# Kernel tuning notes

Hardware: AMD Instinct MI355X
Metric: run time of the kernel (lower is better)

The kernel has to match this reference:

```python
import jax, jax.numpy as jnp
import numpy as np

OUT = 7          # output_size
SR = 2           # sampling_ratio
CANON_SIZE = 224.0
CANON_LVL = 4
MIN_LVL, MAX_LVL = 2, 5
SCALES = (0.25, 0.125, 0.0625, 0.03125)
IMG = 1024.0


def _roi_align(feat, batch_idx, boxes, scale):
    """ROIAlign aligned=True. feat [B,C,H,W], boxes [R,4] (x1,y1,x2,y2) in image coords.
    Returns [R,C,OUT,OUT]."""
    B, C, H, W = feat.shape
    R = boxes.shape[0]
    x1 = boxes[:, 0] * scale - 0.5
    y1 = boxes[:, 1] * scale - 0.5
    x2 = boxes[:, 2] * scale - 0.5
    y2 = boxes[:, 3] * scale - 0.5
    bin_w = (x2 - x1) / OUT
    bin_h = (y2 - y1) / OUT
    S = OUT * SR
    # sample positions in bin units: bin p, sub-sample i -> p + (i+0.5)/SR
    g = (jnp.arange(S, dtype=feat.dtype) + 0.5) / SR
    ys = y1[:, None] + g[None, :] * bin_h[:, None]   # [R,S]
    xs = x1[:, None] + g[None, :] * bin_w[:, None]   # [R,S]
    vy = (ys >= -1.0) & (ys <= H)
    vx = (xs >= -1.0) & (xs <= W)
    yc = jnp.clip(ys, 0.0, H - 1)
    xc = jnp.clip(xs, 0.0, W - 1)
    y0 = jnp.floor(yc).astype(jnp.int32)
    x0 = jnp.floor(xc).astype(jnp.int32)
    y1i = jnp.minimum(y0 + 1, H - 1)
    x1i = jnp.minimum(x0 + 1, W - 1)
    ly = yc - y0.astype(feat.dtype); hy = 1.0 - ly
    lx = xc - x0.astype(feat.dtype); hx = 1.0 - lx
    f = jnp.transpose(feat, (0, 2, 3, 1))            # [B,H,W,C]
    b = batch_idx[:, None, None]                     # [R,1,1]

    def gather(yi, xi):
        # advanced indexing broadcast -> [R,S,S,C]
        return f[b, yi[:, :, None], xi[:, None, :], :]

    def w2(wy, wx):
        return (wy[:, :, None] * wx[:, None, :])[..., None]

    v = (gather(y0, x0) * w2(hy, hx)
         + gather(y0, x1i) * w2(hy, lx)
         + gather(y1i, x0) * w2(ly, hx)
         + gather(y1i, x1i) * w2(ly, lx))             # [R,S,S,C]
    mask = (vy[:, :, None] & vx[:, None, :])[..., None]
    v = jnp.where(mask, v, jnp.zeros((), feat.dtype))
    v = v.reshape(R, OUT, SR, OUT, SR, C).mean(axis=(2, 4))  # avg over SRxSR samples
    return jnp.transpose(v, (0, 3, 1, 2))            # [R,C,OUT,OUT]


def setup_inputs() -> dict:
    key = jax.random.key(0)
    k2, k3, k4, k5, kwh, kc = jax.random.split(key, 6)
    B, C, N = 2, 256, 256
    x2 = jax.random.normal(k2, (B, C, 256, 256), jnp.float32)
    x3 = jax.random.normal(k3, (B, C, 128, 128), jnp.float32)
    x4 = jax.random.normal(k4, (B, C, 64, 64), jnp.float32)
    x5 = jax.random.normal(k5, (B, C, 32, 32), jnp.float32)
    wh = jax.random.uniform(kwh, (B, N, 2), jnp.float32, 32.0, 480.0)
    cxy = jax.random.uniform(kc, (B, N, 2), jnp.float32, 0.0, IMG)
    p1 = jnp.clip(cxy - wh / 2, 0.0, IMG)
    p2 = jnp.clip(cxy + wh / 2, 0.0, IMG)
    boxes = jnp.concatenate([p1, p2], axis=-1)  # [B,N,4] = (x1,y1,x2,y2)
    return {"x2": x2, "x3": x3, "x4": x4, "x5": x5, "boxes": boxes}


def reference(x2, x3, x4, x5, boxes):
    B, N, _ = boxes.shape
    flat = boxes.reshape(B * N, 4)
    batch_idx = jnp.repeat(jnp.arange(B, dtype=jnp.int32), N)
    # FPN level assignment
    area = (flat[:, 2] - flat[:, 0]) * (flat[:, 3] - flat[:, 1])
    sizes = jnp.sqrt(area)
    lvl = jnp.floor(CANON_LVL + jnp.log2(sizes / CANON_SIZE + 1e-8))
    lvl = jnp.clip(lvl, MIN_LVL, MAX_LVL).astype(jnp.int32) - MIN_LVL  # [R] in {0..3}
    feats = (x2, x3, x4, x5)
    C = x2.shape[1]
    out = jnp.zeros((B * N, C, OUT, OUT), x2.dtype)
    for l, (f, s) in enumerate(zip(feats, SCALES)):
        pooled = _roi_align(f, batch_idx, flat, s)
        out = jnp.where((lvl == l)[:, None, None, None], pooled, out)
    return out
```

## Files before the change

### kernel.cpp

```cpp
#include <hip/hip_runtime.h>


#define OUTD 7
#define SRD  2
#define SD   14
#define CCH  256
#define NBOX 256
#define NC   4
#define NCHK (CCH / NC)
#define CAPU 345
#define CAPF (CAPU * 4)
#define NBIN (OUTD * OUTD)

typedef __attribute__((address_space(1))) unsigned int gu32;
typedef __attribute__((address_space(3))) unsigned int lu32;

__device__ __forceinline__ void gl2lds16(const float* g, float* l) {
    __builtin_amdgcn_global_load_lds((gu32*)(unsigned long long)g, (lu32*)l, 16, 0, 0);
}

__global__ __launch_bounds__(256) void roi_direct(
    const float* __restrict__ f0, const float* __restrict__ f1,
    const float* __restrict__ f2, const float* __restrict__ f3,
    const float* __restrict__ boxes, float* __restrict__ out)
{
    const int roi = blockIdx.x;
    const int c0  = blockIdx.y * NC;
    const int t   = threadIdx.x;
    const int b   = roi / NBOX;

    const float bx1 = boxes[roi * 4 + 0];
    const float by1 = boxes[roi * 4 + 1];
    const float bx2 = boxes[roi * 4 + 2];
    const float by2 = boxes[roi * 4 + 3];

    const float area = (bx2 - bx1) * (by2 - by1);
    const float sz   = sqrtf(area);
    int lvl = (int)floorf(4.0f + log2f(sz * (1.0f / 224.0f) + 1e-8f));
    lvl = min(max(lvl, 2), 5) - 2;

    const int   wsh   = 8 - lvl;
    const int   H     = 1 << wsh;
    const int   W     = H;
    const float scale = 1.0f / (float)(4 << lvl);
    const size_t HW   = (size_t)1 << (2 * wsh);

    const float* f  = (lvl == 0) ? f0 : (lvl == 1) ? f1 : (lvl == 2) ? f2 : f3;
    const float* fb = f + (size_t)b * CCH * HW;

    __shared__ int   s_ax0[SD], s_ax1[SD], s_ay0[SD], s_ay1[SD];
    __shared__ float s_wxh[SD], s_wxl[SD], s_wyh[SD], s_wyl[SD];
    __shared__ __align__(16) float s_win[NC * CAPF];

    if (t < SD) {
        const int i = t;
        const float x1r = bx1 * scale - 0.5f;
        const float y1r = by1 * scale - 0.5f;
        const float x2r = bx2 * scale - 0.5f;
        const float y2r = by2 * scale - 0.5f;
        const float bw = (x2r - x1r) * (1.0f / OUTD);
        const float bh = (y2r - y1r) * (1.0f / OUTD);
        const float g  = ((float)i + 0.5f) * (1.0f / SRD);
        const float ys = y1r + g * bh;
        const float xs = x1r + g * bw;
        const float vy = ((ys >= -1.0f) && (ys <= (float)H)) ? 1.0f : 0.0f;
        const float vx = ((xs >= -1.0f) && (xs <= (float)W)) ? 1.0f : 0.0f;
        const float yc = fminf(fmaxf(ys, 0.0f), (float)(H - 1));
        const float xc = fminf(fmaxf(xs, 0.0f), (float)(W - 1));
        const int y0 = (int)yc;
        const int x0 = (int)xc;
        const float ly = yc - (float)y0;
        const float lx = xc - (float)x0;
        s_ay0[i] = y0;
        s_ay1[i] = min(y0 + 1, H - 1);
        s_ax0[i] = x0;
        s_ax1[i] = min(x0 + 1, W - 1);
        s_wyh[i] = vy * (1.0f - ly);
        s_wyl[i] = vy * ly;
        s_wxh[i] = vx * (1.0f - lx);
        s_wxl[i] = vx * lx;
    }
    __syncthreads();

    const int y_lo = s_ay0[0];
    const int y_hi = s_ay1[SD - 1];
    const int x_lo = s_ax0[0] & ~3;
    const int x_hi = s_ax1[SD - 1];
    const int W4 = (x_hi - x_lo + 4) >> 2;
    const int Hw = y_hi - y_lo + 1;
    const int L4 = Hw * W4;

    const int ci  = t / NBIN;
    const int bin = t - ci * NBIN;
    const int oy  = bin / 7;
    const int ox  = bin - oy * 7;
    const int ia = 2 * oy, ib = ia + 1;
    const int ja = 2 * ox, jb = ja + 1;

    float* ob = out + (size_t)roi * (CCH * NBIN) + (size_t)c0 * NBIN;

    if (L4 <= CAPU) {
        const float invW4 = 1.0f / (float)W4;
        const int wv = t >> 6, ln = t & 63;
        const unsigned int gmax = (512u << (2 * wsh)) - 4u;
        const unsigned int wbase = ((unsigned int)y_lo << wsh) + (unsigned int)x_lo;
        for (int c = 0; c < NC; ++c) {
            const unsigned int ch_base =
                (((unsigned int)(b * CCH + c0 + c)) << (2 * wsh)) + wbase;
            float* lb = s_win + c * CAPF;
            for (int o0 = ((wv + c) & 3) << 6; o0 < L4; o0 += 256) {
                const int u = o0 + ln;
                if (u < L4) {
                    int y  = (int)((float)u * invW4);
                    int x4 = u - y * W4;
                    if (x4 < 0)        { x4 += W4; --y; }
                    else if (x4 >= W4) { x4 -= W4; ++y; }
                    unsigned int g = ch_base + ((unsigned int)y << wsh) + ((unsigned int)x4 << 2);
                    g = min(g, gmax);
                    gl2lds16(f + g, lb + (o0 << 2));
                }
            }
        }
        __syncthreads();

        if (t < NC * NBIN) {
            const int rs = W4 << 2;
            const int ryA0 = (s_ay0[ia] - y_lo) * rs, ryA1 = (s_ay1[ia] - y_lo) * rs;
            const int ryB0 = (s_ay0[ib] - y_lo) * rs, ryB1 = (s_ay1[ib] - y_lo) * rs;
            const int rxA0 = s_ax0[ja] - x_lo,        rxA1 = s_ax1[ja] - x_lo;
            const int rxB0 = s_ax0[jb] - x_lo,        rxB1 = s_ax1[jb] - x_lo;
            const float wyAh = s_wyh[ia], wyAl = s_wyl[ia];
            const float wyBh = s_wyh[ib], wyBl = s_wyl[ib];
            const float wxAh = s_wxh[ja], wxAl = s_wxl[ja];
            const float wxBh = s_wxh[jb], wxBl = s_wxl[jb];
            const float* w = s_win + ci * CAPF;
            const float acc =
                wyAh * (wxAh * w[ryA0 + rxA0] + wxAl * w[ryA0 + rxA1])
              + wyAl * (wxAh * w[ryA1 + rxA0] + wxAl * w[ryA1 + rxA1])
              + wyAh * (wxBh * w[ryA0 + rxB0] + wxBl * w[ryA0 + rxB1])
              + wyAl * (wxBh * w[ryA1 + rxB0] + wxBl * w[ryA1 + rxB1])
              + wyBh * (wxAh * w[ryB0 + rxA0] + wxAl * w[ryB0 + rxA1])
              + wyBl * (wxAh * w[ryB1 + rxA0] + wxAl * w[ryB1 + rxA1])
              + wyBh * (wxBh * w[ryB0 + rxB0] + wxBl * w[ryB0 + rxB1])
              + wyBl * (wxBh * w[ryB1 + rxB0] + wxBl * w[ryB1 + rxB1]);
            ob[t] = acc * 0.25f;
        }
    } else {
        if (t < NC * NBIN) {
            const float* fc = fb + (size_t)(c0 + ci) * HW;
            const float acc =
                s_wyh[ia] * (s_wxh[ja] * fc[s_ay0[ia] * W + s_ax0[ja]] + s_wxl[ja] * fc[s_ay0[ia] * W + s_ax1[ja]])
              + s_wyl[ia] * (s_wxh[ja] * fc[s_ay1[ia] * W + s_ax0[ja]] + s_wxl[ja] * fc[s_ay1[ia] * W + s_ax1[ja]])
              + s_wyh[ia] * (s_wxh[jb] * fc[s_ay0[ia] * W + s_ax0[jb]] + s_wxl[jb] * fc[s_ay0[ia] * W + s_ax1[jb]])
              + s_wyl[ia] * (s_wxh[jb] * fc[s_ay1[ia] * W + s_ax0[jb]] + s_wxl[jb] * fc[s_ay1[ia] * W + s_ax1[jb]])
              + s_wyh[ib] * (s_wxh[ja] * fc[s_ay0[ib] * W + s_ax0[ja]] + s_wxl[ja] * fc[s_ay0[ib] * W + s_ax1[ja]])
              + s_wyl[ib] * (s_wxh[ja] * fc[s_ay1[ib] * W + s_ax0[ja]] + s_wxl[ja] * fc[s_ay1[ib] * W + s_ax1[ja]])
              + s_wyh[ib] * (s_wxh[jb] * fc[s_ay0[ib] * W + s_ax0[jb]] + s_wxl[jb] * fc[s_ay0[ib] * W + s_ax1[jb]])
              + s_wyl[ib] * (s_wxh[jb] * fc[s_ay1[ib] * W + s_ax0[jb]] + s_wxl[jb] * fc[s_ay1[ib] * W + s_ax1[jb]]);
            ob[t] = acc * 0.25f;
        }
    }
}

extern "C" void kernel_launch(void* const* d_in, const int* in_sizes, int n_in,
                              void* d_out, int out_size, void* d_ws, size_t ws_size,
                              hipStream_t stream) {
    const float* f0    = (const float*)d_in[0];
    const float* f1    = (const float*)d_in[1];
    const float* f2    = (const float*)d_in[2];
    const float* f3    = (const float*)d_in[3];
    const float* boxes = (const float*)d_in[4];
    float*       outp  = (float*)d_out;

    const int R = out_size / (CCH * NBIN);
    roi_direct<<<dim3(R, NCHK), 256, 0, stream>>>(f0, f1, f2, f3, boxes, outp);
}
```

Measured before the change: 263.6 us.

## Process 16 channels per block with smaller LDS window and no sync

Raises channels per block from 4 to 16 and shrinks the LDS window capacity so up to 128 float4 loads per channel are issued from precomputed offsets. The window bounds are now computed redundantly in every thread, which removes one barrier. The fallback path computes sample coordinates inline instead of reading shared tables. This cuts the grid size and amortises per-block setup across more channels. In exchange, fewer ROIs fit in the LDS path and more of them take the direct global-gather path.

```diff
diff --git a/kernel.cpp b/kernel.cpp
--- a/kernel.cpp
+++ b/kernel.cpp
@@ -2,15 +2,15 @@
 
 
 #define OUTD 7
-#define SRD  2
 #define SD   14
 #define CCH  256
 #define NBOX 256
-#define NC   4
+#define NC   16
 #define NCHK (CCH / NC)
-#define CAPU 345
+#define CAPU 76
 #define CAPF (CAPU * 4)
 #define NBIN (OUTD * OUTD)
+#define NOUT (NC * NBIN)
 
 typedef __attribute__((address_space(1))) unsigned int gu32;
 typedef __attribute__((address_space(3))) unsigned int lu32;
@@ -27,7 +27,7 @@
     const int roi = blockIdx.x;
     const int c0  = blockIdx.y * NC;
     const int t   = threadIdx.x;
-    const int b   = roi / NBOX;
+    const int b   = roi >> 8;
 
     const float bx1 = boxes[roi * 4 + 0];
     const float by1 = boxes[roi * 4 + 1];
@@ -48,116 +48,135 @@
     const float* f  = (lvl == 0) ? f0 : (lvl == 1) ? f1 : (lvl == 2) ? f2 : f3;
     const float* fb = f + (size_t)b * CCH * HW;
 
-    __shared__ int   s_ax0[SD], s_ax1[SD], s_ay0[SD], s_ay1[SD];
-    __shared__ float s_wxh[SD], s_wxl[SD], s_wyh[SD], s_wyl[SD];
+    __shared__ int2   s_py[SD], s_px[SD];
+    __shared__ float2 s_wy[SD], s_wx[SD];
     __shared__ __align__(16) float s_win[NC * CAPF];
+
+    const float x1r = bx1 * scale - 0.5f;
+    const float y1r = by1 * scale - 0.5f;
+    const float bw  = (bx2 - bx1) * scale * (1.0f / OUTD);
+    const float bh  = (by2 - by1) * scale * (1.0f / OUTD);
+    const float Wm1 = (float)(W - 1);
+
+    const float xs0  = x1r + 0.25f * bw, xs13 = x1r + 6.75f * bw;
+    const float ys0  = y1r + 0.25f * bh, ys13 = y1r + 6.75f * bh;
+    const int xf = (int)fminf(fmaxf(xs0, 0.0f), Wm1);
+    const int yf = (int)fminf(fmaxf(ys0, 0.0f), Wm1);
+    const int xl = min((int)fminf(fmaxf(xs13, 0.0f), Wm1) + 1, W - 1);
+    const int yl = min((int)fminf(fmaxf(ys13, 0.0f), Wm1) + 1, W - 1);
+    const int x_lo = xf & ~3;
+    const int y_lo = yf;
+    const int W4 = (xl - x_lo + 4) >> 2;
+    const int Hw = yl - y_lo + 1;
+    const int L4 = Hw * W4;
+    const int rs = W4 << 2;
 
     if (t < SD) {
         const int i = t;
-        const float x1r = bx1 * scale - 0.5f;
-        const float y1r = by1 * scale - 0.5f;
-        const float x2r = bx2 * scale - 0.5f;
-        const float y2r = by2 * scale - 0.5f;
-        const float bw = (x2r - x1r) * (1.0f / OUTD);
-        const float bh = (y2r - y1r) * (1.0f / OUTD);
-        const float g  = ((float)i + 0.5f) * (1.0f / SRD);
+        const float g  = ((float)i + 0.5f) * 0.5f;
         const float ys = y1r + g * bh;
         const float xs = x1r + g * bw;
         const float vy = ((ys >= -1.0f) && (ys <= (float)H)) ? 1.0f : 0.0f;
         const float vx = ((xs >= -1.0f) && (xs <= (float)W)) ? 1.0f : 0.0f;
-        const float yc = fminf(fmaxf(ys, 0.0f), (float)(H - 1));
-        const float xc = fminf(fmaxf(xs, 0.0f), (float)(W - 1));
+        const float yc = fminf(fmaxf(ys, 0.0f), Wm1);
+        const float xc = fminf(fmaxf(xs, 0.0f), Wm1);
         const int y0 = (int)yc;
         const int x0 = (int)xc;
         const float ly = yc - (float)y0;
         const float lx = xc - (float)x0;
-        s_ay0[i] = y0;
-        s_ay1[i] = min(y0 + 1, H - 1);
-        s_ax0[i] = x0;
-        s_ax1[i] = min(x0 + 1, W - 1);
-        s_wyh[i] = vy * (1.0f - ly);
-        s_wyl[i] = vy * ly;
-        s_wxh[i] = vx * (1.0f - lx);
-        s_wxl[i] = vx * lx;
+        s_py[i] = make_int2((y0 - y_lo) * rs, (min(y0 + 1, H - 1) - y_lo) * rs);
+        s_px[i] = make_int2(x0 - x_lo, min(x0 + 1, W - 1) - x_lo);
+        s_wy[i] = make_float2(vy * (1.0f - ly), vy * ly);
+        s_wx[i] = make_float2(vx * (1.0f - lx), vx * lx);
     }
-    __syncthreads();
-
-    const int y_lo = s_ay0[0];
-    const int y_hi = s_ay1[SD - 1];
-    const int x_lo = s_ax0[0] & ~3;
-    const int x_hi = s_ax1[SD - 1];
-    const int W4 = (x_hi - x_lo + 4) >> 2;
-    const int Hw = y_hi - y_lo + 1;
-    const int L4 = Hw * W4;
-
-    const int ci  = t / NBIN;
-    const int bin = t - ci * NBIN;
-    const int oy  = bin / 7;
-    const int ox  = bin - oy * 7;
-    const int ia = 2 * oy, ib = ia + 1;
-    const int ja = 2 * ox, jb = ja + 1;
 
     float* ob = out + (size_t)roi * (CCH * NBIN) + (size_t)c0 * NBIN;
 
     if (L4 <= CAPU) {
+        const int wv = t >> 6, ln = t & 63;
+        const int nT2 = (L4 > 64) ? 1 : 0;
         const float invW4 = 1.0f / (float)W4;
-        const int wv = t >> 6, ln = t & 63;
-        const unsigned int gmax = (512u << (2 * wsh)) - 4u;
+
+        int yA = (int)((float)ln * invW4);
+        int xA = ln - yA * W4;
+        if (xA < 0) { xA += W4; --yA; } else if (xA >= W4) { xA -= W4; ++yA; }
+        const int offA = (yA << wsh) + (xA << 2);
+        int yB = (int)((float)(ln + 64) * invW4);
+        int xB = (ln + 64) - yB * W4;
+        if (xB < 0) { xB += W4; --yB; } else if (xB >= W4) { xB -= W4; ++yB; }
+        const int offB = (yB << wsh) + (xB << 2);
+
         const unsigned int wbase = ((unsigned int)y_lo << wsh) + (unsigned int)x_lo;
-        for (int c = 0; c < NC; ++c) {
-            const unsigned int ch_base =
-                (((unsigned int)(b * CCH + c0 + c)) << (2 * wsh)) + wbase;
-            float* lb = s_win + c * CAPF;
-            for (int o0 = ((wv + c) & 3) << 6; o0 < L4; o0 += 256) {
-                const int u = o0 + ln;
-                if (u < L4) {
-                    int y  = (int)((float)u * invW4);
-                    int x4 = u - y * W4;
-                    if (x4 < 0)        { x4 += W4; --y; }
-                    else if (x4 >= W4) { x4 -= W4; ++y; }
-                    unsigned int g = ch_base + ((unsigned int)y << wsh) + ((unsigned int)x4 << 2);
-                    g = min(g, gmax);
-                    gl2lds16(f + g, lb + (o0 << 2));
-                }
+        const unsigned int cb0   = ((unsigned int)(b * CCH + c0) << (2 * wsh)) + wbase;
+        const unsigned int gmax  = (512u << (2 * wsh)) - 4u;
+        const int nIt = NC << nT2;
+        for (int it = wv; it < nIt; it += 4) {
+            const int c  = it >> nT2;
+            const int tl = it & nT2;
+            const int off = tl ? offB : offA;
+            if (ln + (tl << 6) < L4) {
+                unsigned int g = cb0 + ((unsigned int)c << (2 * wsh)) + (unsigned int)off;
+                g = min(g, gmax);
+                gl2lds16(f + g, s_win + c * CAPF + (tl << 8));
             }
         }
         __syncthreads();
 
-        if (t < NC * NBIN) {
-            const int rs = W4 << 2;
-            const int ryA0 = (s_ay0[ia] - y_lo) * rs, ryA1 = (s_ay1[ia] - y_lo) * rs;
-            const int ryB0 = (s_ay0[ib] - y_lo) * rs, ryB1 = (s_ay1[ib] - y_lo) * rs;
-            const int rxA0 = s_ax0[ja] - x_lo,        rxA1 = s_ax1[ja] - x_lo;
-            const int rxB0 = s_ax0[jb] - x_lo,        rxB1 = s_ax1[jb] - x_lo;
-            const float wyAh = s_wyh[ia], wyAl = s_wyl[ia];
-            const float wyBh = s_wyh[ib], wyBl = s_wyl[ib];
-            const float wxAh = s_wxh[ja], wxAl = s_wxl[ja];
-            const float wxBh = s_wxh[jb], wxBl = s_wxl[jb];
+        for (int idx = t; idx < NOUT; idx += 256) {
+            const int ci  = idx / NBIN;
+            const int bin = idx - ci * NBIN;
+            const int oy  = bin / 7;
+            const int ox  = bin - oy * 7;
+            const int ia = 2 * oy, ib = ia + 1;
+            const int ja = 2 * ox, jb = ja + 1;
+            const int2   pyA = s_py[ia], pyB = s_py[ib];
+            const int2   pxA = s_px[ja], pxB = s_px[jb];
+            const float2 wyA = s_wy[ia], wyB = s_wy[ib];
+            const float2 wxA = s_wx[ja], wxB = s_wx[jb];
             const float* w = s_win + ci * CAPF;
             const float acc =
-                wyAh * (wxAh * w[ryA0 + rxA0] + wxAl * w[ryA0 + rxA1])
-              + wyAl * (wxAh * w[ryA1 + rxA0] + wxAl * w[ryA1 + rxA1])
-              + wyAh * (wxBh * w[ryA0 + rxB0] + wxBl * w[ryA0 + rxB1])
-              + wyAl * (wxBh * w[ryA1 + rxB0] + wxBl * w[ryA1 + rxB1])
-              + wyBh * (wxAh * w[ryB0 + rxA0] + wxAl * w[ryB0 + rxA1])
-              + wyBl * (wxAh * w[ryB1 + rxA0] + wxAl * w[ryB1 + rxA1])
-              + wyBh * (wxBh * w[ryB0 + rxB0] + wxBl * w[ryB0 + rxB1])
-              + wyBl * (wxBh * w[ryB1 + rxB0] + wxBl * w[ryB1 + rxB1]);
-            ob[t] = acc * 0.25f;
+                wyA.x * (wxA.x * w[pyA.x + pxA.x] + wxA.y * w[pyA.x + pxA.y])
+              + wyA.y * (wxA.x * w[pyA.y + pxA.x] + wxA.y * w[pyA.y + pxA.y])
+              + wyA.x * (wxB.x * w[pyA.x + pxB.x] + wxB.y * w[pyA.x + pxB.y])
+              + wyA.y * (wxB.x * w[pyA.y + pxB.x] + wxB.y * w[pyA.y + pxB.y])
+              + wyB.x * (wxA.x * w[pyB.x + pxA.x] + wxA.y * w[pyB.x + pxA.y])
+              + wyB.y * (wxA.x * w[pyB.y + pxA.x] + wxA.y * w[pyB.y + pxA.y])
+              + wyB.x * (wxB.x * w[pyB.x + pxB.x] + wxB.y * w[pyB.x + pxB.y])
+              + wyB.y * (wxB.x * w[pyB.y + pxB.x] + wxB.y * w[pyB.y + pxB.y]);
+            ob[idx] = acc * 0.25f;
         }
     } else {
-        if (t < NC * NBIN) {
+        for (int idx = t; idx < NOUT; idx += 256) {
+            const int ci  = idx / NBIN;
+            const int bin = idx - ci * NBIN;
+            const int oy  = bin / 7;
+            const int ox  = bin - oy * 7;
             const float* fc = fb + (size_t)(c0 + ci) * HW;
-            const float acc =
-                s_wyh[ia] * (s_wxh[ja] * fc[s_ay0[ia] * W + s_ax0[ja]] + s_wxl[ja] * fc[s_ay0[ia] * W + s_ax1[ja]])
-              + s_wyl[ia] * (s_wxh[ja] * fc[s_ay1[ia] * W + s_ax0[ja]] + s_wxl[ja] * fc[s_ay1[ia] * W + s_ax1[ja]])
-              + s_wyh[ia] * (s_wxh[jb] * fc[s_ay0[ia] * W + s_ax0[jb]] + s_wxl[jb] * fc[s_ay0[ia] * W + s_ax1[jb]])
-              + s_wyl[ia] * (s_wxh[jb] * fc[s_ay1[ia] * W + s_ax0[jb]] + s_wxl[jb] * fc[s_ay1[ia] * W + s_ax1[jb]])
-              + s_wyh[ib] * (s_wxh[ja] * fc[s_ay0[ib] * W + s_ax0[ja]] + s_wxl[ja] * fc[s_ay0[ib] * W + s_ax1[ja]])
-              + s_wyl[ib] * (s_wxh[ja] * fc[s_ay1[ib] * W + s_ax0[ja]] + s_wxl[ja] * fc[s_ay1[ib] * W + s_ax1[ja]])
-              + s_wyh[ib] * (s_wxh[jb] * fc[s_ay0[ib] * W + s_ax0[jb]] + s_wxl[jb] * fc[s_ay0[ib] * W + s_ax1[jb]])
-              + s_wyl[ib] * (s_wxh[jb] * fc[s_ay1[ib] * W + s_ax0[jb]] + s_wxl[jb] * fc[s_ay1[ib] * W + s_ax1[jb]]);
-            ob[t] = acc * 0.25f;
+            float acc = 0.0f;
+            #pragma unroll
+            for (int sy = 0; sy < 2; ++sy) {
+                const float gy = ((float)(2 * oy + sy) + 0.5f) * 0.5f;
+                const float ys = y1r + gy * bh;
+                const float vy = ((ys >= -1.0f) && (ys <= (float)H)) ? 1.0f : 0.0f;
+                const float yc = fminf(fmaxf(ys, 0.0f), Wm1);
+                const int   yy0 = (int)yc;
+                const int   yy1 = min(yy0 + 1, H - 1);
+                const float ly = yc - (float)yy0;
+                #pragma unroll
+                for (int sx = 0; sx < 2; ++sx) {
+                    const float gx = ((float)(2 * ox + sx) + 0.5f) * 0.5f;
+                    const float xs = x1r + gx * bw;
+                    const float vx = ((xs >= -1.0f) && (xs <= (float)W)) ? 1.0f : 0.0f;
+                    const float xc = fminf(fmaxf(xs, 0.0f), Wm1);
+                    const int   xx0 = (int)xc;
+                    const int   xx1 = min(xx0 + 1, W - 1);
+                    const float lx = xc - (float)xx0;
+                    acc += vy * vx *
+                        ((1.0f - ly) * ((1.0f - lx) * fc[yy0 * W + xx0] + lx * fc[yy0 * W + xx1])
+                       +         ly  * ((1.0f - lx) * fc[yy1 * W + xx0] + lx * fc[yy1 * W + xx1]));
+                }
+            }
+            ob[idx] = acc * 0.25f;
         }
     }
 }
```

Result: slower. 324.2 us (+23.0%).

## Make each wavefront own one channel and drop block-wide barriers

Applied to the files above, without the earlier changes.

Each of the four wavefronts now loads and reduces its own channel's window, so the block-level __syncthreads calls are replaced by a per-wave vmcnt wait. Sample coordinates and weights are computed per lane in registers, and the window bounds come from a closed form, which removes the shared coordinate tables and the first barrier. LDS capacity per channel drops, so more ROIs fall to the slow global-gather path, while lower LDS use may allow more resident blocks. Relying on the vmcnt wait for global_load_lds visibility within a wave is a subtle correctness assumption.

```diff
diff --git a/kernel.cpp b/kernel.cpp
--- a/kernel.cpp
+++ b/kernel.cpp
@@ -2,13 +2,11 @@
 
 
 #define OUTD 7
-#define SRD  2
-#define SD   14
 #define CCH  256
 #define NBOX 256
 #define NC   4
 #define NCHK (CCH / NC)
-#define CAPU 345
+#define CAPU 300
 #define CAPF (CAPU * 4)
 #define NBIN (OUTD * OUTD)
 
@@ -25,9 +23,11 @@
     const float* __restrict__ boxes, float* __restrict__ out)
 {
     const int roi = blockIdx.x;
-    const int c0  = blockIdx.y * NC;
     const int t   = threadIdx.x;
-    const int b   = roi / NBOX;
+    const int wv  = t >> 6;
+    const int ln  = t & 63;
+    const int c   = blockIdx.y * NC + wv;
+    const int b   = roi >> 8;
 
     const float bx1 = boxes[roi * 4 + 0];
     const float by1 = boxes[roi * 4 + 1];
@@ -43,122 +43,117 @@
     const int   H     = 1 << wsh;
     const int   W     = H;
     const float scale = 1.0f / (float)(4 << lvl);
-    const size_t HW   = (size_t)1 << (2 * wsh);
+    const float* f = (lvl == 0) ? f0 : (lvl == 1) ? f1 : (lvl == 2) ? f2 : f3;
 
-    const float* f  = (lvl == 0) ? f0 : (lvl == 1) ? f1 : (lvl == 2) ? f2 : f3;
-    const float* fb = f + (size_t)b * CCH * HW;
+    const float x1r = bx1 * scale - 0.5f;
+    const float y1r = by1 * scale - 0.5f;
+    const float bw  = (bx2 - bx1) * scale * (1.0f / OUTD);
+    const float bh  = (by2 - by1) * scale * (1.0f / OUTD);
+    const float Wm1 = (float)(W - 1);
 
-    __shared__ int   s_ax0[SD], s_ax1[SD], s_ay0[SD], s_ay1[SD];
-    __shared__ float s_wxh[SD], s_wxl[SD], s_wyh[SD], s_wyl[SD];
+    const int xf = (int)fminf(fmaxf(x1r + 0.25f * bw, 0.0f), Wm1);
+    const int yf = (int)fminf(fmaxf(y1r + 0.25f * bh, 0.0f), Wm1);
+    const int xl = min((int)fminf(fmaxf(x1r + 6.75f * bw, 0.0f), Wm1) + 1, W - 1);
+    const int yl = min((int)fminf(fmaxf(y1r + 6.75f * bh, 0.0f), Wm1) + 1, W - 1);
+    const int x_lo = xf & ~3;
+    const int y_lo = yf;
+    const int W4 = (xl - x_lo + 4) >> 2;
+    const int Hw = yl - y_lo + 1;
+    const int L4 = Hw * W4;
+    const int rs = W4 << 2;
+
     __shared__ __align__(16) float s_win[NC * CAPF];
 
-    if (t < SD) {
-        const int i = t;
-        const float x1r = bx1 * scale - 0.5f;
-        const float y1r = by1 * scale - 0.5f;
-        const float x2r = bx2 * scale - 0.5f;
-        const float y2r = by2 * scale - 0.5f;
-        const float bw = (x2r - x1r) * (1.0f / OUTD);
-        const float bh = (y2r - y1r) * (1.0f / OUTD);
-        const float g  = ((float)i + 0.5f) * (1.0f / SRD);
-        const float ys = y1r + g * bh;
-        const float xs = x1r + g * bw;
-        const float vy = ((ys >= -1.0f) && (ys <= (float)H)) ? 1.0f : 0.0f;
-        const float vx = ((xs >= -1.0f) && (xs <= (float)W)) ? 1.0f : 0.0f;
-        const float yc = fminf(fmaxf(ys, 0.0f), (float)(H - 1));
-        const float xc = fminf(fmaxf(xs, 0.0f), (float)(W - 1));
-        const int y0 = (int)yc;
-        const int x0 = (int)xc;
-        const float ly = yc - (float)y0;
-        const float lx = xc - (float)x0;
-        s_ay0[i] = y0;
-        s_ay1[i] = min(y0 + 1, H - 1);
-        s_ax0[i] = x0;
-        s_ax1[i] = min(x0 + 1, W - 1);
-        s_wyh[i] = vy * (1.0f - ly);
-        s_wyl[i] = vy * ly;
-        s_wxh[i] = vx * (1.0f - lx);
-        s_wxl[i] = vx * lx;
-    }
-    __syncthreads();
+    const bool fast = (L4 <= CAPU);
 
-    const int y_lo = s_ay0[0];
-    const int y_hi = s_ay1[SD - 1];
-    const int x_lo = s_ax0[0] & ~3;
-    const int x_hi = s_ax1[SD - 1];
-    const int W4 = (x_hi - x_lo + 4) >> 2;
-    const int Hw = y_hi - y_lo + 1;
-    const int L4 = Hw * W4;
-
-    const int ci  = t / NBIN;
-    const int bin = t - ci * NBIN;
-    const int oy  = bin / 7;
-    const int ox  = bin - oy * 7;
-    const int ia = 2 * oy, ib = ia + 1;
-    const int ja = 2 * ox, jb = ja + 1;
-
-    float* ob = out + (size_t)roi * (CCH * NBIN) + (size_t)c0 * NBIN;
-
-    if (L4 <= CAPU) {
+    const unsigned int cbase = ((unsigned int)(b * CCH + c)) << (2 * wsh);
+    if (fast) {
+        const unsigned int wbase = ((unsigned int)y_lo << wsh) + (unsigned int)x_lo;
+        const unsigned int gmax  = (512u << (2 * wsh)) - 4u;
         const float invW4 = 1.0f / (float)W4;
-        const int wv = t >> 6, ln = t & 63;
-        const unsigned int gmax = (512u << (2 * wsh)) - 4u;
-        const unsigned int wbase = ((unsigned int)y_lo << wsh) + (unsigned int)x_lo;
-        for (int c = 0; c < NC; ++c) {
-            const unsigned int ch_base =
-                (((unsigned int)(b * CCH + c0 + c)) << (2 * wsh)) + wbase;
-            float* lb = s_win + c * CAPF;
-            for (int o0 = ((wv + c) & 3) << 6; o0 < L4; o0 += 256) {
-                const int u = o0 + ln;
-                if (u < L4) {
-                    int y  = (int)((float)u * invW4);
-                    int x4 = u - y * W4;
-                    if (x4 < 0)        { x4 += W4; --y; }
-                    else if (x4 >= W4) { x4 -= W4; ++y; }
-                    unsigned int g = ch_base + ((unsigned int)y << wsh) + ((unsigned int)x4 << 2);
-                    g = min(g, gmax);
-                    gl2lds16(f + g, lb + (o0 << 2));
-                }
+        float* lb = s_win + wv * CAPF;
+        for (int o0 = 0; o0 < L4; o0 += 64) {
+            const int u = o0 + ln;
+            if (u < L4) {
+                int y  = (int)((float)u * invW4);
+                int x4 = u - y * W4;
+                if (x4 < 0) { x4 += W4; --y; } else if (x4 >= W4) { x4 -= W4; ++y; }
+                unsigned int g = cbase + wbase + ((unsigned int)y << wsh) + ((unsigned int)x4 << 2);
+                g = min(g, gmax);
+                gl2lds16(f + g, lb + (o0 << 2));
             }
         }
-        __syncthreads();
+    }
 
-        if (t < NC * NBIN) {
-            const int rs = W4 << 2;
-            const int ryA0 = (s_ay0[ia] - y_lo) * rs, ryA1 = (s_ay1[ia] - y_lo) * rs;
-            const int ryB0 = (s_ay0[ib] - y_lo) * rs, ryB1 = (s_ay1[ib] - y_lo) * rs;
-            const int rxA0 = s_ax0[ja] - x_lo,        rxA1 = s_ax1[ja] - x_lo;
-            const int rxB0 = s_ax0[jb] - x_lo,        rxB1 = s_ax1[jb] - x_lo;
-            const float wyAh = s_wyh[ia], wyAl = s_wyl[ia];
-            const float wyBh = s_wyh[ib], wyBl = s_wyl[ib];
-            const float wxAh = s_wxh[ja], wxAl = s_wxl[ja];
-            const float wxBh = s_wxh[jb], wxBl = s_wxl[jb];
-            const float* w = s_win + ci * CAPF;
-            const float acc =
-                wyAh * (wxAh * w[ryA0 + rxA0] + wxAl * w[ryA0 + rxA1])
-              + wyAl * (wxAh * w[ryA1 + rxA0] + wxAl * w[ryA1 + rxA1])
-              + wyAh * (wxBh * w[ryA0 + rxB0] + wxBl * w[ryA0 + rxB1])
-              + wyAl * (wxBh * w[ryA1 + rxB0] + wxBl * w[ryA1 + rxB1])
-              + wyBh * (wxAh * w[ryB0 + rxA0] + wxAl * w[ryB0 + rxA1])
-              + wyBl * (wxAh * w[ryB1 + rxA0] + wxAl * w[ryB1 + rxA1])
-              + wyBh * (wxBh * w[ryB0 + rxB0] + wxBl * w[ryB0 + rxB1])
-              + wyBl * (wxBh * w[ryB1 + rxB0] + wxBl * w[ryB1 + rxB1]);
-            ob[t] = acc * 0.25f;
-        }
+    const int l  = min(ln, 48);
+    const int oy = l / 7;
+    const int ox = l - oy * 7;
+
+    const float ysA = y1r + ((float)(2 * oy) + 0.5f) * 0.5f * bh;
+    const float ysB = y1r + ((float)(2 * oy + 1) + 0.5f) * 0.5f * bh;
+    const float xsA = x1r + ((float)(2 * ox) + 0.5f) * 0.5f * bw;
+    const float xsB = x1r + ((float)(2 * ox + 1) + 0.5f) * 0.5f * bw;
+
+    const float vyA = ((ysA >= -1.0f) && (ysA <= (float)H)) ? 1.0f : 0.0f;
+    const float vyB = ((ysB >= -1.0f) && (ysB <= (float)H)) ? 1.0f : 0.0f;
+    const float vxA = ((xsA >= -1.0f) && (xsA <= (float)W)) ? 1.0f : 0.0f;
+    const float vxB = ((xsB >= -1.0f) && (xsB <= (float)W)) ? 1.0f : 0.0f;
+
+    const float ycA = fminf(fmaxf(ysA, 0.0f), Wm1);
+    const float ycB = fminf(fmaxf(ysB, 0.0f), Wm1);
+    const float xcA = fminf(fmaxf(xsA, 0.0f), Wm1);
+    const float xcB = fminf(fmaxf(xsB, 0.0f), Wm1);
+
+    const int yA0 = (int)ycA, yB0 = (int)ycB;
+    const int xA0 = (int)xcA, xB0 = (int)xcB;
+    const int yA1 = min(yA0 + 1, H - 1), yB1 = min(yB0 + 1, H - 1);
+    const int xA1 = min(xA0 + 1, W - 1), xB1 = min(xB0 + 1, W - 1);
+
+    const float lyA = ycA - (float)yA0, lyB = ycB - (float)yB0;
+    const float lxA = xcA - (float)xA0, lxB = xcB - (float)xB0;
+
+    const float wyAh = vyA * (1.0f - lyA), wyAl = vyA * lyA;
+    const float wyBh = vyB * (1.0f - lyB), wyBl = vyB * lyB;
+    const float wxAh = vxA * (1.0f - lxA), wxAl = vxA * lxA;
+    const float wxBh = vxB * (1.0f - lxB), wxBl = vxB * lxB;
+
+    float acc;
+    if (fast) {
+        const int ryA0 = (yA0 - y_lo) * rs, ryA1 = (yA1 - y_lo) * rs;
+        const int ryB0 = (yB0 - y_lo) * rs, ryB1 = (yB1 - y_lo) * rs;
+        const int rxA0 = xA0 - x_lo, rxA1 = xA1 - x_lo;
+        const int rxB0 = xB0 - x_lo, rxB1 = xB1 - x_lo;
+
+        asm volatile("s_waitcnt vmcnt(0)" ::: "memory");
+        __builtin_amdgcn_sched_barrier(0);
+
+        const float* w = s_win + wv * CAPF;
+        acc =
+            wyAh * (wxAh * w[ryA0 + rxA0] + wxAl * w[ryA0 + rxA1])
+          + wyAl * (wxAh * w[ryA1 + rxA0] + wxAl * w[ryA1 + rxA1])
+          + wyAh * (wxBh * w[ryA0 + rxB0] + wxBl * w[ryA0 + rxB1])
+          + wyAl * (wxBh * w[ryA1 + rxB0] + wxBl * w[ryA1 + rxB1])
+          + wyBh * (wxAh * w[ryB0 + rxA0] + wxAl * w[ryB0 + rxA1])
+          + wyBl * (wxAh * w[ryB1 + rxA0] + wxAl * w[ryB1 + rxA1])
+          + wyBh * (wxBh * w[ryB0 + rxB0] + wxBl * w[ryB0 + rxB1])
+          + wyBl * (wxBh * w[ryB1 + rxB0] + wxBl * w[ryB1 + rxB1]);
     } else {
-        if (t < NC * NBIN) {
-            const float* fc = fb + (size_t)(c0 + ci) * HW;
-            const float acc =
-                s_wyh[ia] * (s_wxh[ja] * fc[s_ay0[ia] * W + s_ax0[ja]] + s_wxl[ja] * fc[s_ay0[ia] * W + s_ax1[ja]])
-              + s_wyl[ia] * (s_wxh[ja] * fc[s_ay1[ia] * W + s_ax0[ja]] + s_wxl[ja] * fc[s_ay1[ia] * W + s_ax1[ja]])
-              + s_wyh[ia] * (s_wxh[jb] * fc[s_ay0[ia] * W + s_ax0[jb]] + s_wxl[jb] * fc[s_ay0[ia] * W + s_ax1[jb]])
-              + s_wyl[ia] * (s_wxh[jb] * fc[s_ay1[ia] * W + s_ax0[jb]] + s_wxl[jb] * fc[s_ay1[ia] * W + s_ax1[jb]])
-              + s_wyh[ib] * (s_wxh[ja] * fc[s_ay0[ib] * W + s_ax0[ja]] + s_wxl[ja] * fc[s_ay0[ib] * W + s_ax1[ja]])
-              + s_wyl[ib] * (s_wxh[ja] * fc[s_ay1[ib] * W + s_ax0[ja]] + s_wxl[ja] * fc[s_ay1[ib] * W + s_ax1[ja]])
-              + s_wyh[ib] * (s_wxh[jb] * fc[s_ay0[ib] * W + s_ax0[jb]] + s_wxl[jb] * fc[s_ay0[ib] * W + s_ax1[jb]])
-              + s_wyl[ib] * (s_wxh[jb] * fc[s_ay1[ib] * W + s_ax0[jb]] + s_wxl[jb] * fc[s_ay1[ib] * W + s_ax1[jb]]);
-            ob[t] = acc * 0.25f;
-        }
+        const float* fc = f + cbase;
+        const int gA0 = yA0 << wsh, gA1 = yA1 << wsh;
+        const int gB0 = yB0 << wsh, gB1 = yB1 << wsh;
+        acc =
+            wyAh * (wxAh * fc[gA0 + xA0] + wxAl * fc[gA0 + xA1])
+          + wyAl * (wxAh * fc[gA1 + xA0] + wxAl * fc[gA1 + xA1])
+          + wyAh * (wxBh * fc[gA0 + xB0] + wxBl * fc[gA0 + xB1])
+          + wyAl * (wxBh * fc[gA1 + xB0] + wxBl * fc[gA1 + xB1])
+          + wyBh * (wxAh * fc[gB0 + xA0] + wxAl * fc[gB0 + xA1])
+          + wyBl * (wxAh * fc[gB1 + xA0] + wxAl * fc[gB1 + xA1])
+          + wyBh * (wxBh * fc[gB0 + xB0] + wxBl * fc[gB0 + xB1])
+          + wyBl * (wxBh * fc[gB1 + xB0] + wxBl * fc[gB1 + xB1]);
+    }
+
+    if (ln < NBIN) {
+        out[(size_t)roi * (CCH * NBIN) + (size_t)c * NBIN + ln] = acc * 0.25f;
     }
 }
 
```

After: 260.0 us. About the same (-1.4%).
